# Kernel optimization log

Hardware: AMD Instinct MI355X
Metric: run time of the kernel (lower is better)

Reference implementation:

```python
import jax, jax.numpy as jnp
import numpy as np

WORLD_SIZE = 8
M = 8192
K = 8192
N = 8192
LOCAL_K = K // WORLD_SIZE  # 1024


def setup_inputs() -> dict:
    key = jax.random.key(0)
    kx, kw = jax.random.split(key)
    # Per-rank activation shard: [ws, M, local_K]
    x = jax.random.normal(kx, (WORLD_SIZE, M, LOCAL_K), dtype=jnp.float32) * 0.02
    # Per-rank weight shard (K split across ranks): [ws, local_K, N]
    weight = jax.random.normal(kw, (WORLD_SIZE, LOCAL_K, N), dtype=jnp.float32) * 0.02
    return {"x": x, "weight": weight}


def reference(x, weight):
    # Each rank r computes partial = x_r @ W_r : [M, N].
    # reduce_scatter_tensor sums partials over ranks and gives rank r the
    # r-th row-chunk of size M // world_size. Summing over the rank axis via
    # einsum fuses the per-rank GEMMs and the reduction.
    full = jnp.einsum('rmk,rkn->mn', x, weight)  # [M, N] = sum_r x_r @ W_r
    # Stack every rank's scattered output: [ws, M//ws, N]
    return full.reshape(WORLD_SIZE, M // WORLD_SIZE, N)
```

## Files before the change

### kernel.cpp

```cpp
#include <hip/hip_runtime.h>
#include <stdint.h>

#define WSZ 8
#define MD 8192
#define ND 8192
#define KD 8192
#define LK 1024

typedef __attribute__((ext_vector_type(8))) short short8;
typedef __attribute__((ext_vector_type(4))) float f32x4;
typedef __attribute__((ext_vector_type(8))) unsigned short u16x8;

__device__ __forceinline__ unsigned short f2bf(float f) {
  unsigned int u = __float_as_uint(f);
  u += 0x7fffu + ((u >> 16) & 1u);
  return (unsigned short)(u >> 16);
}

__global__ __launch_bounds__(256) void conv_a(const float* __restrict__ x,
                                              unsigned short* __restrict__ A) {
  const size_t total8 = (size_t)WSZ * MD * LK / 8;
  size_t stride = (size_t)gridDim.x * blockDim.x;
  for (size_t idx = (size_t)blockIdx.x * blockDim.x + threadIdx.x; idx < total8; idx += stride) {
    size_t e = idx * 8;
    unsigned int r   = (unsigned int)(e >> 23);
    unsigned int rem = (unsigned int)(e & ((1u << 23) - 1u));
    unsigned int m   = rem >> 10;
    unsigned int k   = rem & 1023u;
    const f32x4* src = (const f32x4*)(x + e);
    f32x4 v0 = src[0], v1 = src[1];
    u16x8 o;
    o[0] = f2bf(v0[0]); o[1] = f2bf(v0[1]); o[2] = f2bf(v0[2]); o[3] = f2bf(v0[3]);
    o[4] = f2bf(v1[0]); o[5] = f2bf(v1[1]); o[6] = f2bf(v1[2]); o[7] = f2bf(v1[3]);
    *(u16x8*)(A + (size_t)m * KD + r * LK + k) = o;
  }
}

__global__ __launch_bounds__(256) void conv_bt(const float* __restrict__ w,
                                               unsigned short* __restrict__ Bt) {
  __shared__ float tile[64][65];
  const int nt = ND / 64;
  int bx = blockIdx.x % nt;
  int by = blockIdx.x / nt;
  int t = threadIdx.x;
  size_t kb = (size_t)by * 64, nb = (size_t)bx * 64;
  {
    int j  = t & 63;
    int i0 = t >> 6;
#pragma unroll
    for (int rep = 0; rep < 16; ++rep) {
      int i = i0 * 16 + rep;
      tile[i][j] = w[(kb + i) * (size_t)ND + nb + j];
    }
  }
  __syncthreads();
  {
    int j2 = (t & 31) * 2;
    int n0 = t >> 5;
#pragma unroll
    for (int rep = 0; rep < 8; ++rep) {
      int n = n0 * 8 + rep;
      unsigned int pair = (unsigned int)f2bf(tile[j2][n]) |
                          ((unsigned int)f2bf(tile[j2 + 1][n]) << 16);
      *(unsigned int*)(Bt + (nb + n) * (size_t)KD + kb + j2) = pair;
    }
  }
}

#define BM 128
#define BN 128
#define BK 32

__global__ __launch_bounds__(256) void gemm_bf16(const unsigned short* __restrict__ A,
                                                 const unsigned short* __restrict__ Bt,
                                                 float* __restrict__ C) {
  __shared__ __align__(16) short As[BM * BK];
  __shared__ __align__(16) short Bs[BN * BK];
  int t = threadIdx.x;
  int lane = t & 63;
  int wid  = t >> 6;

  const int nwg = 64 * 64;
  const int cpx = nwg >> 3;
  int orig = blockIdx.x;
  int wg = (orig & 7) * cpx + (orig >> 3);
  const int GM = 8;
  const int width = GM * 64;
  int group = wg / width;
  int pid_m = group * GM + (wg % GM);
  int pid_n = (wg % width) / GM;

  size_t arow = (size_t)pid_m * BM;
  size_t brow = (size_t)pid_n * BN;

  const unsigned short* ga = A  + (arow + (size_t)(t >> 2)) * KD + (size_t)(t & 3) * 8;
  const unsigned short* gb = Bt + (brow + (size_t)(t >> 2)) * KD + (size_t)(t & 3) * 8;

  int wm = wid >> 1, wn = wid & 1;
  int lr = lane & 15;
  int kg = lane >> 4;

  const short* pa0 = &As[(wm * 64 + lr) * BK + kg * 8];
  const short* pb0 = &Bs[(wn * 64 + lr) * BK + kg * 8];

  f32x4 acc[4][4];
#pragma unroll
  for (int i = 0; i < 4; ++i)
#pragma unroll
    for (int j = 0; j < 4; ++j)
      acc[i][j] = (f32x4){0.f, 0.f, 0.f, 0.f};

  for (int kt = 0; kt < KD / BK; ++kt) {
    const unsigned short* gak = ga + kt * BK;
    const unsigned short* gbk = gb + kt * BK;
    __builtin_amdgcn_global_load_lds(
        (const __attribute__((address_space(1))) unsigned int*)gak,
        (__attribute__((address_space(3))) unsigned int*)&As[t * 8], 16, 0, 0);
    __builtin_amdgcn_global_load_lds(
        (const __attribute__((address_space(1))) unsigned int*)(gak + (size_t)64 * KD),
        (__attribute__((address_space(3))) unsigned int*)&As[2048 + t * 8], 16, 0, 0);
    __builtin_amdgcn_global_load_lds(
        (const __attribute__((address_space(1))) unsigned int*)gbk,
        (__attribute__((address_space(3))) unsigned int*)&Bs[t * 8], 16, 0, 0);
    __builtin_amdgcn_global_load_lds(
        (const __attribute__((address_space(1))) unsigned int*)(gbk + (size_t)64 * KD),
        (__attribute__((address_space(3))) unsigned int*)&Bs[2048 + t * 8], 16, 0, 0);
    __syncthreads();

    short8 af[4], bfr[4];
#pragma unroll
    for (int mi = 0; mi < 4; ++mi) af[mi]  = *(const short8*)(pa0 + mi * 16 * BK);
#pragma unroll
    for (int ni = 0; ni < 4; ++ni) bfr[ni] = *(const short8*)(pb0 + ni * 16 * BK);
#pragma unroll
    for (int mi = 0; mi < 4; ++mi)
#pragma unroll
      for (int ni = 0; ni < 4; ++ni)
        acc[mi][ni] = __builtin_amdgcn_mfma_f32_16x16x32_bf16(af[mi], bfr[ni], acc[mi][ni], 0, 0, 0);
    __syncthreads();
  }

  size_t crow = arow + (size_t)(wm * 64 + kg * 4);
  size_t ccol = brow + (size_t)(wn * 64 + lr);
#pragma unroll
  for (int mi = 0; mi < 4; ++mi) {
#pragma unroll
    for (int ni = 0; ni < 4; ++ni) {
      f32x4 v = acc[mi][ni];
#pragma unroll
      for (int j = 0; j < 4; ++j)
        C[(crow + mi * 16 + j) * ND + ccol + ni * 16] = v[j];
    }
  }
}

extern "C" void kernel_launch(void* const* d_in, const int* in_sizes, int n_in,
                              void* d_out, int out_size, void* d_ws, size_t ws_size,
                              hipStream_t stream) {
  const float* x = (const float*)d_in[0];
  const float* w = (const float*)d_in[1];
  float* out = (float*)d_out;

  unsigned short* Abf = (unsigned short*)d_ws;
  unsigned short* Bbf = Abf + (size_t)MD * KD;

  conv_a<<<4096, 256, 0, stream>>>(x, Abf);
  conv_bt<<<(KD / 64) * (ND / 64), 256, 0, stream>>>(w, Bbf);
  gemm_bf16<<<64 * 64, 256, 0, stream>>>(Abf, Bbf, out);
}
```

Measured before the change: 2.230 ms.

## Use 256x256 GEMM tiles with triple-buffered async LDS pipeline

The GEMM moves to 256x256 output tiles handled by 512 threads (8 waves, each computing 128x64), with a three-stage LDS ring fed by global_load_lds prefetching two k-tiles ahead. Explicit waitcnt and s_barrier replace the two __syncthreads per iteration, and s_setprio raises priority around the MFMA bursts. The goal is more data reuse per global load and overlap of memory traffic with MFMA work. The B-transpose conversion kernel also switches to 16-byte vector stores. In exchange, LDS use (96KB) and register pressure rise, leaving one workgroup per CU, and correctness depends on the hand-written wait counts.

```diff
diff --git a/kernel.cpp b/kernel.cpp
--- a/kernel.cpp
+++ b/kernel.cpp
@@ -55,37 +55,48 @@
   }
   __syncthreads();
   {
-    int j2 = (t & 31) * 2;
-    int n0 = t >> 5;
-#pragma unroll
-    for (int rep = 0; rep < 8; ++rep) {
-      int n = n0 * 8 + rep;
-      unsigned int pair = (unsigned int)f2bf(tile[j2][n]) |
-                          ((unsigned int)f2bf(tile[j2 + 1][n]) << 16);
-      *(unsigned int*)(Bt + (nb + n) * (size_t)KD + kb + j2) = pair;
-    }
-  }
-}
-
-#define BM 128
-#define BN 128
+    int n  = t >> 2;
+    int ks = t & 3;
+#pragma unroll
+    for (int rep = 0; rep < 2; ++rep) {
+      int k8 = ks + rep * 4;
+      u16x8 o;
+#pragma unroll
+      for (int i = 0; i < 8; ++i) o[i] = f2bf(tile[k8 * 8 + i][n]);
+      *(u16x8*)(Bt + (nb + n) * (size_t)KD + kb + k8 * 8) = o;
+    }
+  }
+}
+
+#define BM 256
+#define BN 256
 #define BK 32
-
-__global__ __launch_bounds__(256) void gemm_bf16(const unsigned short* __restrict__ A,
-                                                 const unsigned short* __restrict__ Bt,
-                                                 float* __restrict__ C) {
-  __shared__ __align__(16) short As[BM * BK];
-  __shared__ __align__(16) short Bs[BN * BK];
+#define NT (KD / BK)
+
+#define GLDS(src, dst)                                                           \
+  __builtin_amdgcn_global_load_lds(                                              \
+      (const __attribute__((address_space(1))) unsigned int*)(src),              \
+      (__attribute__((address_space(3))) unsigned int*)(dst), 16, 0, 0)
+
+__global__ __launch_bounds__(512, 1) void gemm_bf16(const unsigned short* __restrict__ A,
+                                                    const unsigned short* __restrict__ Bt,
+                                                    float* __restrict__ C) {
+  __shared__ __align__(16) short As[3][BM * BK];
+  __shared__ __align__(16) short Bs[3][BN * BK];
+
   int t = threadIdx.x;
   int lane = t & 63;
   int wid  = t >> 6;
-
-  const int nwg = 64 * 64;
-  const int cpx = nwg >> 3;
+  int wr = wid >> 2;
+  int wc = wid & 3;
+  int lr = lane & 15;
+  int kg = lane >> 4;
+
+  const int nwg = 32 * 32;
   int orig = blockIdx.x;
-  int wg = (orig & 7) * cpx + (orig >> 3);
+  int wg = (orig & 7) * (nwg >> 3) + (orig >> 3);
   const int GM = 8;
-  const int width = GM * 64;
+  const int width = GM * 32;
   int group = wg / width;
   int pid_m = group * GM + (wg % GM);
   int pid_n = (wg % width) / GM;
@@ -93,57 +104,79 @@
   size_t arow = (size_t)pid_m * BM;
   size_t brow = (size_t)pid_n * BN;
 
-  const unsigned short* ga = A  + (arow + (size_t)(t >> 2)) * KD + (size_t)(t & 3) * 8;
-  const unsigned short* gb = Bt + (brow + (size_t)(t >> 2)) * KD + (size_t)(t & 3) * 8;
-
-  int wm = wid >> 1, wn = wid & 1;
-  int lr = lane & 15;
-  int kg = lane >> 4;
-
-  const short* pa0 = &As[(wm * 64 + lr) * BK + kg * 8];
-  const short* pb0 = &Bs[(wn * 64 + lr) * BK + kg * 8];
-
-  f32x4 acc[4][4];
-#pragma unroll
-  for (int i = 0; i < 4; ++i)
-#pragma unroll
-    for (int j = 0; j < 4; ++j)
-      acc[i][j] = (f32x4){0.f, 0.f, 0.f, 0.f};
-
-  for (int kt = 0; kt < KD / BK; ++kt) {
-    const unsigned short* gak = ga + kt * BK;
-    const unsigned short* gbk = gb + kt * BK;
-    __builtin_amdgcn_global_load_lds(
-        (const __attribute__((address_space(1))) unsigned int*)gak,
-        (__attribute__((address_space(3))) unsigned int*)&As[t * 8], 16, 0, 0);
-    __builtin_amdgcn_global_load_lds(
-        (const __attribute__((address_space(1))) unsigned int*)(gak + (size_t)64 * KD),
-        (__attribute__((address_space(3))) unsigned int*)&As[2048 + t * 8], 16, 0, 0);
-    __builtin_amdgcn_global_load_lds(
-        (const __attribute__((address_space(1))) unsigned int*)gbk,
-        (__attribute__((address_space(3))) unsigned int*)&Bs[t * 8], 16, 0, 0);
-    __builtin_amdgcn_global_load_lds(
-        (const __attribute__((address_space(1))) unsigned int*)(gbk + (size_t)64 * KD),
-        (__attribute__((address_space(3))) unsigned int*)&Bs[2048 + t * 8], 16, 0, 0);
-    __syncthreads();
-
-    short8 af[4], bfr[4];
-#pragma unroll
-    for (int mi = 0; mi < 4; ++mi) af[mi]  = *(const short8*)(pa0 + mi * 16 * BK);
-#pragma unroll
-    for (int ni = 0; ni < 4; ++ni) bfr[ni] = *(const short8*)(pb0 + ni * 16 * BK);
+  const unsigned short* pA = A  + (arow + (size_t)(t >> 2)) * KD + (size_t)(t & 3) * 8;
+  const unsigned short* pB = Bt + (brow + (size_t)(t >> 2)) * KD + (size_t)(t & 3) * 8;
+
+  const int aoff = (wr * 128 + lr) * BK + kg * 8;
+  const int boff = (wc * 64 + lr) * BK + kg * 8;
+
+  f32x4 acc[8][4];
+#pragma unroll
+  for (int i = 0; i < 8; ++i)
+#pragma unroll
+    for (int j = 0; j < 4; ++j) acc[i][j] = (f32x4){0.f, 0.f, 0.f, 0.f};
+
+  auto stage = [&](int kt, int b) {
+    const unsigned short* sa = pA + (size_t)kt * BK;
+    const unsigned short* sb = pB + (size_t)kt * BK;
+    GLDS(sa,                    &As[b][t * 8]);
+    GLDS(sa + (size_t)128 * KD, &As[b][4096 + t * 8]);
+    GLDS(sb,                    &Bs[b][t * 8]);
+    GLDS(sb + (size_t)128 * KD, &Bs[b][4096 + t * 8]);
+  };
+
+  stage(0, 0);
+  stage(1, 1);
+  asm volatile("s_waitcnt vmcnt(4)" ::: "memory");
+  asm volatile("s_barrier" ::: "memory");
+
+  int cur = 0;
+  for (int kt = 0; kt < NT; ++kt) {
+    int pre = cur + 2; if (pre >= 3) pre -= 3;
+    if (kt + 2 < NT) stage(kt + 2, pre);
+
+    const short* Ac = &As[cur][0];
+    const short* Bc = &Bs[cur][0];
+
+    short8 af[4], bf[4];
+#pragma unroll
+    for (int mi = 0; mi < 4; ++mi) af[mi] = *(const short8*)(Ac + aoff + mi * 16 * BK);
+#pragma unroll
+    for (int ni = 0; ni < 4; ++ni) bf[ni] = *(const short8*)(Bc + boff + ni * 16 * BK);
+    __builtin_amdgcn_s_setprio(1);
 #pragma unroll
     for (int mi = 0; mi < 4; ++mi)
 #pragma unroll
       for (int ni = 0; ni < 4; ++ni)
-        acc[mi][ni] = __builtin_amdgcn_mfma_f32_16x16x32_bf16(af[mi], bfr[ni], acc[mi][ni], 0, 0, 0);
-    __syncthreads();
-  }
-
-  size_t crow = arow + (size_t)(wm * 64 + kg * 4);
-  size_t ccol = brow + (size_t)(wn * 64 + lr);
-#pragma unroll
-  for (int mi = 0; mi < 4; ++mi) {
+        acc[mi][ni] = __builtin_amdgcn_mfma_f32_16x16x32_bf16(af[mi], bf[ni], acc[mi][ni], 0, 0, 0);
+    __builtin_amdgcn_s_setprio(0);
+
+    short8 ag[4];
+#pragma unroll
+    for (int mi = 0; mi < 4; ++mi) ag[mi] = *(const short8*)(Ac + aoff + (4 + mi) * 16 * BK);
+    __builtin_amdgcn_s_setprio(1);
+#pragma unroll
+    for (int mi = 0; mi < 4; ++mi)
+#pragma unroll
+      for (int ni = 0; ni < 4; ++ni)
+        acc[4 + mi][ni] = __builtin_amdgcn_mfma_f32_16x16x32_bf16(ag[mi], bf[ni], acc[4 + mi][ni], 0, 0, 0);
+    __builtin_amdgcn_s_setprio(0);
+
+    asm volatile("s_waitcnt lgkmcnt(0)" ::: "memory");
+    if (kt < NT - 2) {
+      asm volatile("s_waitcnt vmcnt(4)" ::: "memory");
+    } else {
+      asm volatile("s_waitcnt vmcnt(0)" ::: "memory");
+    }
+    asm volatile("s_barrier" ::: "memory");
+
+    cur = cur + 1; if (cur >= 3) cur = 0;
+  }
+
+  size_t crow = arow + (size_t)(wr * 128 + kg * 4);
+  size_t ccol = brow + (size_t)(wc * 64 + lr);
+#pragma unroll
+  for (int mi = 0; mi < 8; ++mi) {
 #pragma unroll
     for (int ni = 0; ni < 4; ++ni) {
       f32x4 v = acc[mi][ni];
@@ -166,5 +199,5 @@
 
   conv_a<<<4096, 256, 0, stream>>>(x, Abf);
   conv_bt<<<(KD / 64) * (ND / 64), 256, 0, stream>>>(w, Bbf);
-  gemm_bf16<<<64 * 64, 256, 0, stream>>>(Abf, Bbf, out);
-}
+  gemm_bf16<<<32 * 32, 512, 0, stream>>>(Abf, Bbf, out);
+}
```

New measurement: 1.999 ms. 1.12x faster.
